# Kernel tuning notes

Measured on AMD Instinct MI355X. Metric: run time of the kernel, lower is better.

The kernel has to match this reference:

```python
import jax, jax.numpy as jnp
import numpy as np

D_MODEL, D_FF, D_NEURON, N_HEADS = 1024, 4096, 128, 8
HEAD_DIM = D_NEURON // N_HEADS
LN_EPS = 1e-5

def gelu(x):
    return jax.nn.gelu(x, approximate=False)  # torch default is exact erf GELU

def setup_inputs() -> dict:
    key = jax.random.key(0)
    ks = jax.random.split(key, 16)
    s = 0.02
    inp = {
        "x": jax.random.normal(ks[0], (2, 2048, D_MODEL), jnp.float32),
        "neuron_patterns": jax.random.normal(ks[1], (D_FF, D_MODEL), jnp.float32) * s,
        "neuron_vecs": jax.random.normal(ks[2], (D_FF, D_NEURON), jnp.float32) * s,
        "neuron_out_dirs": jax.random.normal(ks[3], (D_FF, D_MODEL), jnp.float32) * s,
        "router_w1": jax.random.normal(ks[4], (D_MODEL, D_MODEL), jnp.float32) * s,
        "router_w2": jax.random.normal(ks[5], (D_FF, D_MODEL), jnp.float32) * s,
        "ln_g": jnp.ones((D_MODEL,), jnp.float32),
        "ln_b": jnp.zeros((D_MODEL,), jnp.float32),
        "in_proj_w": jax.random.normal(ks[6], (3 * D_NEURON, D_NEURON), jnp.float32) * s,
        "in_proj_b": jnp.zeros((3 * D_NEURON,), jnp.float32),
        "out_proj_w": jax.random.normal(ks[7], (D_NEURON, D_NEURON), jnp.float32) * s,
        "out_proj_b": jnp.zeros((D_NEURON,), jnp.float32),
        "wp1_w": jax.random.normal(ks[8], (D_NEURON // 2, D_NEURON), jnp.float32) * s,
        "wp1_b": jnp.zeros((D_NEURON // 2,), jnp.float32),
        "wp2_w": jax.random.normal(ks[9], (1, D_NEURON // 2), jnp.float32) * s,
        "wp2_b": jnp.zeros((1,), jnp.float32),
        "top_k": 32,
    }
    return inp

def _forward(x, neuron_patterns, neuron_vecs, neuron_out_dirs, router_w1, router_w2,
             ln_g, ln_b, in_proj_w, in_proj_b, out_proj_w, out_proj_b,
             wp1_w, wp1_b, wp2_w, wp2_b, top_k):
    B, S, D = x.shape
    xf = x.reshape(-1, D)                                  # [N, D]
    # Router (MLP): LayerNorm -> gelu(x @ W1^T) -> @ W2^T
    mu = jnp.mean(xf, axis=-1, keepdims=True)
    var = jnp.mean(jnp.square(xf - mu), axis=-1, keepdims=True)
    xn = (xf - mu) * jax.lax.rsqrt(var + LN_EPS) * ln_g + ln_b
    h = gelu(xn @ router_w1.T)
    scores = h @ router_w2.T                               # [N, d_ff]
    _, idx = jax.lax.top_k(scores, top_k)                  # [N, k]
    pats = neuron_patterns[idx]                            # [N, k, D]
    sems = neuron_vecs[idx]                                # [N, k, dn]
    dirs = neuron_out_dirs[idx]                            # [N, k, D]
    base = gelu(jnp.einsum('nd,nkd->nk', xf, pats))        # [N, k]
    # Small self-attention over the k gathered neuron semantics (eval: no dropout)
    qkv = sems @ in_proj_w.T + in_proj_b                   # [N, k, 3*dn]
    q, kk, v = jnp.split(qkv, 3, axis=-1)
    N, K = q.shape[0], q.shape[1]
    q = q.reshape(N, K, N_HEADS, HEAD_DIM)
    kk = kk.reshape(N, K, N_HEADS, HEAD_DIM)
    v = v.reshape(N, K, N_HEADS, HEAD_DIM)
    att = jnp.einsum('nqhd,nkhd->nhqk', q, kk) / jnp.sqrt(jnp.float32(HEAD_DIM))
    att = jax.nn.softmax(att, axis=-1)
    ao = jnp.einsum('nhqk,nkhd->nqhd', att, v).reshape(N, K, D_NEURON)
    attended = ao @ out_proj_w.T + out_proj_b              # [N, k, dn]
    # Gate: sigmoid(MLP(attended)) -> [N, k, 1]
    sw = jax.nn.sigmoid(gelu(attended @ wp1_w.T + wp1_b) @ wp2_w.T + wp2_b)
    final = base[..., None] * sw                           # [N, k, 1]
    out = jnp.einsum('nko,nkd->nd', final, dirs)           # sum over k neurons
    return out.reshape(B, S, D)

def reference(x, neuron_patterns, neuron_vecs, neuron_out_dirs, router_w1, router_w2,
              ln_g, ln_b, in_proj_w, in_proj_b, out_proj_w, out_proj_b,
              wp1_w, wp1_b, wp2_w, wp2_b, top_k):
    return _forward(x, neuron_patterns, neuron_vecs, neuron_out_dirs, router_w1, router_w2,
                    ln_g, ln_b, in_proj_w, in_proj_b, out_proj_w, out_proj_b,
                    wp1_w, wp1_b, wp2_w, wp2_b, top_k)
```

## Files before the change

kernel.cpp:

```cpp
#include <hip/hip_runtime.h>
#include <math.h>

#define N_TOK 4096
#define DM 1024
#define DFF 4096
#define DN 128
#define NH 8
#define HD 16
#define KSEL 32
#define KCAND 48
#define KMAX 64

typedef __attribute__((ext_vector_type(4))) float floatx4;
typedef __attribute__((ext_vector_type(8))) short short8;
typedef __attribute__((ext_vector_type(8))) unsigned short ushort8v;
typedef __attribute__((ext_vector_type(4))) unsigned short ushort4v;

__device__ __forceinline__ float gelu_f(float x) {
  return 0.5f * x * (1.0f + erff(x * 0.70710678118654752440f));
}
__device__ __forceinline__ float bf2f(unsigned short u) {
  union { unsigned int i; float f; } v; v.i = ((unsigned int)u) << 16; return v.f;
}
__device__ __forceinline__ unsigned short f2bf(float f) {
  unsigned int x = __float_as_uint(f);
  unsigned int r = (x + 0x7fffu + ((x >> 16) & 1u)) >> 16;
  return (unsigned short)r;
}
__device__ __forceinline__ void split3(float v, unsigned short& h, unsigned short& m,
                                       unsigned short& lo) {
  h = f2bf(v);
  float r1 = v - bf2f(h);
  m = f2bf(r1);
  float r2 = r1 - bf2f(m);
  lo = f2bf(r2);
}

__global__ __launch_bounds__(256) void ln3_kernel(const float* __restrict__ x,
    const float* __restrict__ g, const float* __restrict__ b,
    unsigned short* __restrict__ xh, unsigned short* __restrict__ xm,
    unsigned short* __restrict__ xl) {
  int n = blockIdx.x, tid = threadIdx.x;
  const float* row = x + (size_t)n * DM;
  float s = 0.f, sq = 0.f;
  for (int i = tid; i < DM; i += 256) { float v = row[i]; s += v; sq += v * v; }
  for (int off = 32; off; off >>= 1) { s += __shfl_down(s, off); sq += __shfl_down(sq, off); }
  __shared__ float ss[4], ssq[4];
  __shared__ float s_mu, s_rs;
  int wid = tid >> 6;
  if ((tid & 63) == 0) { ss[wid] = s; ssq[wid] = sq; }
  __syncthreads();
  if (tid == 0) {
    float S = ss[0] + ss[1] + ss[2] + ss[3];
    float Q = ssq[0] + ssq[1] + ssq[2] + ssq[3];
    float mu = S * (1.f / DM);
    float var = Q * (1.f / DM) - mu * mu;
    s_mu = mu; s_rs = rsqrtf(var + 1e-5f);
  }
  __syncthreads();
  float mu = s_mu, rs = s_rs;
  size_t base = (size_t)n * DM;
  for (int i = tid; i < DM; i += 256) {
    float v = (row[i] - mu) * rs * g[i] + b[i];
    unsigned short h, m, lo;
    split3(v, h, m, lo);
    xh[base + i] = h; xm[base + i] = m; xl[base + i] = lo;
  }
}

__global__ __launch_bounds__(256) void cvt_split3(const float* __restrict__ in,
    unsigned short* __restrict__ oh, unsigned short* __restrict__ om,
    unsigned short* __restrict__ ol) {
  int i = (blockIdx.x * 256 + threadIdx.x) * 4;
  float4 v = *(const float4*)(in + i);
  unsigned short h0, m0, l0, h1, m1, l1, h2, m2, l2, h3, m3, l3;
  split3(v.x, h0, m0, l0);
  split3(v.y, h1, m1, l1);
  split3(v.z, h2, m2, l2);
  split3(v.w, h3, m3, l3);
  ushort4v hh = {h0, h1, h2, h3};
  ushort4v mm = {m0, m1, m2, m3};
  ushort4v ll = {l0, l1, l2, l3};
  *(ushort4v*)(oh + i) = hh;
  *(ushort4v*)(om + i) = mm;
  *(ushort4v*)(ol + i) = ll;
}

__global__ __launch_bounds__(256) void cvt_bf16(const float* __restrict__ in,
    unsigned short* __restrict__ out) {
  int i = (blockIdx.x * 256 + threadIdx.x) * 4;
  float4 v = *(const float4*)(in + i);
  ushort4v o = {f2bf(v.x), f2bf(v.y), f2bf(v.z), f2bf(v.w)};
  *(ushort4v*)(out + i) = o;
}

__global__ __launch_bounds__(256, 1) void gemm1s(
    const unsigned short* __restrict__ Ah_, const unsigned short* __restrict__ Am_,
    const unsigned short* __restrict__ Al_, const unsigned short* __restrict__ Bh_,
    const unsigned short* __restrict__ Bm_, const unsigned short* __restrict__ Bl_,
    float* __restrict__ H, unsigned short* __restrict__ Hb) {
  __shared__ short Ahs[128 * 32], Ams[128 * 32], Als[128 * 32];
  __shared__ short Bhs[128 * 32], Bms[128 * 32], Bls[128 * 32];
  const int K = 1024;
  const int N = DM;
  int tid = threadIdx.x;
  int w = tid >> 6, l = tid & 63;
  size_t brow = (size_t)blockIdx.y * 128;
  size_t bcol = (size_t)blockIdx.x * 128;

  int r0 = w * 32 + (l >> 2);
  int g0 = (l & 3) ^ ((r0 >> 1) & 3);
  size_t oA0 = (brow + r0) * (size_t)K + g0 * 8;
  size_t oA1 = (brow + r0 + 16) * (size_t)K + g0 * 8;
  size_t oB0 = (bcol + r0) * (size_t)K + g0 * 8;
  size_t oB1 = (bcol + r0 + 16) * (size_t)K + g0 * 8;
  const short* gAh0 = (const short*)Ah_ + oA0; const short* gAh1 = (const short*)Ah_ + oA1;
  const short* gAm0 = (const short*)Am_ + oA0; const short* gAm1 = (const short*)Am_ + oA1;
  const short* gAl0 = (const short*)Al_ + oA0; const short* gAl1 = (const short*)Al_ + oA1;
  const short* gBh0 = (const short*)Bh_ + oB0; const short* gBh1 = (const short*)Bh_ + oB1;
  const short* gBm0 = (const short*)Bm_ + oB0; const short* gBm1 = (const short*)Bm_ + oB1;
  const short* gBl0 = (const short*)Bl_ + oB0; const short* gBl1 = (const short*)Bl_ + oB1;
  short* lAh = &Ahs[w * 1024]; short* lAm = &Ams[w * 1024]; short* lAl = &Als[w * 1024];
  short* lBh = &Bhs[w * 1024]; short* lBm = &Bms[w * 1024]; short* lBl = &Bls[w * 1024];

  const short8 *pah[4], *pam[4], *pal[4], *pbh[4], *pbm[4], *pbl[4];
#pragma unroll
  for (int i = 0; i < 4; i++) {
    int m = (w >> 1) * 64 + i * 16 + (l & 15);
    int slot = m * 4 + ((l >> 4) ^ ((m >> 1) & 3));
    pah[i] = (const short8*)&Ahs[slot * 8];
    pam[i] = (const short8*)&Ams[slot * 8];
    pal[i] = (const short8*)&Als[slot * 8];
    int nn = (w & 1) * 64 + i * 16 + (l & 15);
    int slotb = nn * 4 + ((l >> 4) ^ ((nn >> 1) & 3));
    pbh[i] = (const short8*)&Bhs[slotb * 8];
    pbm[i] = (const short8*)&Bms[slotb * 8];
    pbl[i] = (const short8*)&Bls[slotb * 8];
  }

  floatx4 acc[4][4];
#pragma unroll
  for (int i = 0; i < 4; i++)
#pragma unroll
    for (int j = 0; j < 4; j++) acc[i][j] = (floatx4){0.f, 0.f, 0.f, 0.f};

#define GLD(GP, LB) \
  __builtin_amdgcn_global_load_lds((const __attribute__((address_space(1))) unsigned int*)(GP), \
                                   (__attribute__((address_space(3))) unsigned int*)(LB), 16, 0, 0)

  for (int k0 = 0; k0 < K; k0 += 32) {
    __syncthreads();
    GLD(gAh0 + k0, lAh); GLD(gAh1 + k0, lAh + 512);
    GLD(gAm0 + k0, lAm); GLD(gAm1 + k0, lAm + 512);
    GLD(gAl0 + k0, lAl); GLD(gAl1 + k0, lAl + 512);
    GLD(gBh0 + k0, lBh); GLD(gBh1 + k0, lBh + 512);
    GLD(gBm0 + k0, lBm); GLD(gBm1 + k0, lBm + 512);
    GLD(gBl0 + k0, lBl); GLD(gBl1 + k0, lBl + 512);
    __syncthreads();
    short8 ah[4], am[4], al[4], bh[4], bm[4], bl[4];
#pragma unroll
    for (int i = 0; i < 4; i++) {
      ah[i] = *pah[i]; am[i] = *pam[i]; al[i] = *pal[i];
      bh[i] = *pbh[i]; bm[i] = *pbm[i]; bl[i] = *pbl[i];
    }
#pragma unroll
    for (int i = 0; i < 4; i++)
#pragma unroll
      for (int j = 0; j < 4; j++)
        acc[i][j] = __builtin_amdgcn_mfma_f32_16x16x32_bf16(ah[i], bh[j], acc[i][j], 0, 0, 0);
#pragma unroll
    for (int i = 0; i < 4; i++)
#pragma unroll
      for (int j = 0; j < 4; j++)
        acc[i][j] = __builtin_amdgcn_mfma_f32_16x16x32_bf16(am[i], bh[j], acc[i][j], 0, 0, 0);
#pragma unroll
    for (int i = 0; i < 4; i++)
#pragma unroll
      for (int j = 0; j < 4; j++)
        acc[i][j] = __builtin_amdgcn_mfma_f32_16x16x32_bf16(ah[i], bm[j], acc[i][j], 0, 0, 0);
#pragma unroll
    for (int i = 0; i < 4; i++)
#pragma unroll
      for (int j = 0; j < 4; j++)
        acc[i][j] = __builtin_amdgcn_mfma_f32_16x16x32_bf16(al[i], bh[j], acc[i][j], 0, 0, 0);
#pragma unroll
    for (int i = 0; i < 4; i++)
#pragma unroll
      for (int j = 0; j < 4; j++)
        acc[i][j] = __builtin_amdgcn_mfma_f32_16x16x32_bf16(ah[i], bl[j], acc[i][j], 0, 0, 0);
#pragma unroll
    for (int i = 0; i < 4; i++)
#pragma unroll
      for (int j = 0; j < 4; j++)
        acc[i][j] = __builtin_amdgcn_mfma_f32_16x16x32_bf16(am[i], bm[j], acc[i][j], 0, 0, 0);
  }
#undef GLD

#pragma unroll
  for (int i = 0; i < 4; i++) {
#pragma unroll
    for (int j = 0; j < 4; j++) {
#pragma unroll
      for (int r = 0; r < 4; r++) {
        size_t row = brow + (w >> 1) * 64 + i * 16 + (l >> 4) * 4 + r;
        size_t col = bcol + (w & 1) * 64 + j * 16 + (l & 15);
        float v = gelu_f(acc[i][j][r]);
        H[row * N + col] = v;
        Hb[row * N + col] = f2bf(v);
      }
    }
  }
}

__global__ __launch_bounds__(256) void gemm_bf(const unsigned short* __restrict__ Ah,
    const unsigned short* __restrict__ Bh, unsigned short* __restrict__ C) {
  __shared__ short Asd[128 * 32];
  __shared__ short Bsd[128 * 32];
  const int K = 1024;
  int tid = threadIdx.x;
  int w = tid >> 6, l = tid & 63;
  size_t brow = (size_t)blockIdx.y * 128;
  size_t bcol = (size_t)blockIdx.x * 128;
  const short* Ab = (const short*)Ah + brow * K;
  const short* Bb = (const short*)Bh + bcol * K;

  int r0 = w * 32 + (l >> 2);
  int g0 = (l & 3) ^ ((r0 >> 1) & 3);
  const short* Ag0 = Ab + (size_t)r0 * K + g0 * 8;
  const short* Ag1 = Ab + (size_t)(r0 + 16) * K + g0 * 8;
  const short* Bg0 = Bb + (size_t)r0 * K + g0 * 8;
  const short* Bg1 = Bb + (size_t)(r0 + 16) * K + g0 * 8;
  short* ALds0 = &Asd[w * 1024];
  short* ALds1 = &Asd[w * 1024 + 512];
  short* BLds0 = &Bsd[w * 1024];
  short* BLds1 = &Bsd[w * 1024 + 512];

  const short8* aptr[4];
  const short8* bptr[4];
#pragma unroll
  for (int i = 0; i < 4; i++) {
    int m = (w >> 1) * 64 + i * 16 + (l & 15);
    int slot = m * 4 + ((l >> 4) ^ ((m >> 1) & 3));
    aptr[i] = (const short8*)&Asd[slot * 8];
    int n = (w & 1) * 64 + i * 16 + (l & 15);
    int slotb = n * 4 + ((l >> 4) ^ ((n >> 1) & 3));
    bptr[i] = (const short8*)&Bsd[slotb * 8];
  }

  floatx4 acc[4][4];
#pragma unroll
  for (int i = 0; i < 4; i++)
#pragma unroll
    for (int j = 0; j < 4; j++) acc[i][j] = (floatx4){0.f, 0.f, 0.f, 0.f};

  for (int k0 = 0; k0 < K; k0 += 32) {
    __syncthreads();
    __builtin_amdgcn_global_load_lds((const __attribute__((address_space(1))) unsigned int*)(Ag0 + k0),
                                     (__attribute__((address_space(3))) unsigned int*)ALds0, 16, 0, 0);
    __builtin_amdgcn_global_load_lds((const __attribute__((address_space(1))) unsigned int*)(Ag1 + k0),
                                     (__attribute__((address_space(3))) unsigned int*)ALds1, 16, 0, 0);
    __builtin_amdgcn_global_load_lds((const __attribute__((address_space(1))) unsigned int*)(Bg0 + k0),
                                     (__attribute__((address_space(3))) unsigned int*)BLds0, 16, 0, 0);
    __builtin_amdgcn_global_load_lds((const __attribute__((address_space(1))) unsigned int*)(Bg1 + k0),
                                     (__attribute__((address_space(3))) unsigned int*)BLds1, 16, 0, 0);
    __syncthreads();
    short8 a[4], b[4];
#pragma unroll
    for (int i = 0; i < 4; i++) a[i] = *aptr[i];
#pragma unroll
    for (int j = 0; j < 4; j++) b[j] = *bptr[j];
#pragma unroll
    for (int i = 0; i < 4; i++)
#pragma unroll
      for (int j = 0; j < 4; j++)
        acc[i][j] = __builtin_amdgcn_mfma_f32_16x16x32_bf16(a[i], b[j], acc[i][j], 0, 0, 0);
  }

#pragma unroll
  for (int i = 0; i < 4; i++) {
#pragma unroll
    for (int j = 0; j < 4; j++) {
#pragma unroll
      for (int r = 0; r < 4; r++) {
        size_t row = brow + (w >> 1) * 64 + i * 16 + (l >> 4) * 4 + r;
        size_t col = bcol + (w & 1) * 64 + j * 16 + (l & 15);
        C[row * DFF + col] = f2bf(acc[i][j][r]);
      }
    }
  }
}

__global__ __launch_bounds__(256) void topk2_kernel(const unsigned short* __restrict__ scores,
    int* __restrict__ cand, int* __restrict__ cnt) {
  int wv = threadIdx.x >> 6, l = threadIdx.x & 63;
  int n = blockIdx.x * 4 + wv;
  const ushort8v* row = (const ushort8v*)(scores + (size_t)n * DFF);
  unsigned short key[64];
#pragma unroll
  for (int i = 0; i < 8; i++) {
    ushort8v v = row[l * 8 + i];
#pragma unroll
    for (int e = 0; e < 8; e++) {
      unsigned short u = v[e];
      key[i * 8 + e] = (u & 0x8000u) ? (unsigned short)(~u)
                                     : (unsigned short)(u | 0x8000u);
    }
  }
  unsigned int prefix = 0;
#pragma unroll
  for (int bit = 15; bit >= 0; bit--) {
    unsigned int probe = prefix | (1u << bit);
    int c = 0;
#pragma unroll
    for (int i = 0; i < 64; i++) c += (key[i] >= probe) ? 1 : 0;
#pragma unroll
    for (int s = 1; s < 64; s <<= 1) c += __shfl_xor(c, s);
    if (c >= KCAND) prefix = probe;
  }
  unsigned short thr = (unsigned short)prefix;
  unsigned long long ltmask = (1ull << l) - 1ull;
  int base = 0;
  int* outp = cand + (size_t)n * KMAX;
#pragma unroll
  for (int i = 0; i < 64; i++) {
    bool p = key[i] >= thr;
    unsigned long long m = __ballot(p);
    if (p) {
      int pos = base + __popcll(m & ltmask);
      if (pos < KMAX) outp[pos] = l * 64 + i;
    }
    base += __popcll(m);
  }
  if (l == 0) cnt[n] = base < KMAX ? base : KMAX;
}

__global__ __launch_bounds__(256) void rescore_kernel(const float* __restrict__ h,
    const float* __restrict__ w2f, const int* __restrict__ cand,
    const int* __restrict__ cnt, int* __restrict__ idx32) {
  __shared__ float sh[DM];
  __shared__ float sc[KMAX];
  __shared__ int sidx[KMAX];
  __shared__ int s_cnt;
  int n = blockIdx.x, tid = threadIdx.x;
  *(float4*)&sh[tid * 4] = *(const float4*)(h + (size_t)n * DM + tid * 4);
  if (tid == 0) s_cnt = cnt[n];
  if (tid < KMAX) { sidx[tid] = cand[(size_t)n * KMAX + tid]; sc[tid] = -INFINITY; }
  __syncthreads();
  int cntv = s_cnt;
  int w = tid >> 6, lane = tid & 63;
  for (int c = w; c < cntv; c += 4) {
    const float4* row = (const float4*)(w2f + (size_t)sidx[c] * DM);
    const float4* hp = (const float4*)sh;
    float s = 0.f;
#pragma unroll
    for (int t = 0; t < 4; t++) {
      float4 wv = row[t * 64 + lane];
      float4 hv = hp[t * 64 + lane];
      s = fmaf(wv.x, hv.x, s); s = fmaf(wv.y, hv.y, s);
      s = fmaf(wv.z, hv.z, s); s = fmaf(wv.w, hv.w, s);
    }
    for (int off = 32; off; off >>= 1) s += __shfl_xor(s, off);
    if (lane == 0) sc[c] = s;
  }
  __syncthreads();
  if (tid < cntv) {
    float st = sc[tid]; int it = sidx[tid];
    int rank = 0;
    for (int j = 0; j < KMAX; j++) {
      float sj = sc[j];
      rank += (sj > st) || (sj == st && sidx[j] < it);
    }
    if (rank < KSEL) idx32[(size_t)n * KSEL + rank] = it;
  }
}

__global__ __launch_bounds__(384) void qkvtab_kernel(const float* __restrict__ nv,
    const float* __restrict__ ipw, const float* __restrict__ ipb,
    unsigned short* __restrict__ tab) {
  __shared__ float s_nv[8 * 128];
  int f0 = blockIdx.x * 8;
  int tid = threadIdx.x;
  for (int i = tid; i < 8 * 128; i += 384) s_nv[i] = nv[(size_t)f0 * 128 + i];
  __syncthreads();
  int row = tid;
  float bias = ipb[row];
  float acc[8];
#pragma unroll
  for (int ff = 0; ff < 8; ff++) acc[ff] = bias;
  const float* wr = ipw + (size_t)row * 128;
  for (int c = 0; c < 128; c++) {
    float w = wr[c];
#pragma unroll
    for (int ff = 0; ff < 8; ff++) acc[ff] = fmaf(s_nv[ff * 128 + c], w, acc[ff]);
  }
#pragma unroll
  for (int ff = 0; ff < 8; ff++) tab[(size_t)(f0 + ff) * 384 + row] = f2bf(acc[ff]);
}

#define AOS 132
__global__ __launch_bounds__(256) void tail4_kernel(
    const float* __restrict__ xf, const float* __restrict__ pats,
    const float* __restrict__ dirs, const unsigned short* __restrict__ qtab_b,
    const int* __restrict__ idxs,
    const unsigned short* __restrict__ opwb, const float* __restrict__ opb,
    const unsigned short* __restrict__ w1b, const float* __restrict__ b1,
    const float* __restrict__ w2, const float* __restrict__ b2,
    float* __restrict__ out) {
  __shared__ unsigned short s_kv[2 * 32 * 128];
  __shared__ float s_x[1024];
  __shared__ unsigned short s_ao[32 * AOS];
  __shared__ float s_base[32];
  __shared__ float s_coef[32];
  __shared__ int s_idx[32];
  unsigned short* s_k = s_kv;
  unsigned short* s_v = s_kv + 32 * 128;
  unsigned short* s_at = s_kv;

  int n = blockIdx.x, tid = threadIdx.x;
  int w = tid >> 6, l = tid & 63;

  if (tid < 32) s_idx[tid] = idxs[(size_t)n * 32 + tid];
  *(float4*)&s_x[tid * 4] = *(const float4*)(xf + (size_t)n * DM + tid * 4);
  __syncthreads();

#pragma unroll
  for (int p = 0; p < 4; p++) {
    int i = p * 256 + tid;
    int j = i >> 5, c = i & 31;
    int half = c >> 4, cc = c & 15;
    ushort8v v = *(const ushort8v*)(qtab_b + (size_t)s_idx[j] * 384 + 128 + half * 128 + cc * 8);
    *(ushort8v*)&s_kv[half * 4096 + j * 128 + cc * 8] = v;
  }

  {
    int j = tid >> 3, g = tid & 7;
    const float4* pr = (const float4*)(pats + (size_t)s_idx[j] * DM);
    const float4* xp = (const float4*)s_x;
    float s = 0.f;
#pragma unroll 8
    for (int it = 0; it < 32; it++) {
      float4 pv = pr[it * 8 + g];
      float4 xv = xp[it * 8 + g];
      s = fmaf(pv.x, xv.x, s); s = fmaf(pv.y, xv.y, s);
      s = fmaf(pv.z, xv.z, s); s = fmaf(pv.w, xv.w, s);
    }
    s += __shfl_xor(s, 1);
    s += __shfl_xor(s, 2);
    s += __shfl_xor(s, 4);
    if (g == 0) s_base[j] = gelu_f(s);
  }
  __syncthreads();

  {
    int qj = l & 31;
    int h0 = w * 2 + (l >> 5);
    const ushort8v* qr = (const ushort8v*)(qtab_b + (size_t)s_idx[qj] * 384 + h0 * 16);
    ushort8v q0 = qr[0], q1 = qr[1];
    float q[16];
#pragma unroll
    for (int e = 0; e < 8; e++) { q[e] = bf2f(q0[e]); q[8 + e] = bf2f(q1[e]); }
    float att[32];
#pragma unroll 8
    for (int kj = 0; kj < 32; kj++) {
      const ushort8v* kr = (const ushort8v*)&s_k[kj * 128 + h0 * 16];
      ushort8v k0 = kr[0], k1 = kr[1];
      float s = 0.f;
#pragma unroll
      for (int e = 0; e < 8; e++) s = fmaf(q[e], bf2f(k0[e]), s);
#pragma unroll
      for (int e = 0; e < 8; e++) s = fmaf(q[8 + e], bf2f(k1[e]), s);
      att[kj] = s * 0.25f;
    }
    float m = att[0];
#pragma unroll
    for (int k = 1; k < 32; k++) m = fmaxf(m, att[k]);
    float sum = 0.f;
#pragma unroll
    for (int k = 0; k < 32; k++) { att[k] = expf(att[k] - m); sum += att[k]; }
    float inv = 1.f / sum;
#pragma unroll
    for (int k = 0; k < 32; k++) att[k] *= inv;
    float o[16];
#pragma unroll
    for (int e = 0; e < 16; e++) o[e] = 0.f;
#pragma unroll 8
    for (int kj = 0; kj < 32; kj++) {
      const ushort8v* vr = (const ushort8v*)&s_v[kj * 128 + h0 * 16];
      ushort8v v0 = vr[0], v1 = vr[1];
      float a = att[kj];
#pragma unroll
      for (int e = 0; e < 8; e++) o[e] = fmaf(a, bf2f(v0[e]), o[e]);
#pragma unroll
      for (int e = 0; e < 8; e++) o[8 + e] = fmaf(a, bf2f(v1[e]), o[8 + e]);
    }
    ushort8v o0, o1;
#pragma unroll
    for (int e = 0; e < 8; e++) { o0[e] = f2bf(o[e]); o1[e] = f2bf(o[8 + e]); }
    ushort8v* ao = (ushort8v*)&s_ao[qj * AOS + h0 * 16];
    ao[0] = o0; ao[1] = o1;
  }
  __syncthreads();

  {
    floatx4 acc[4];
#pragma unroll
    for (int nt = 0; nt < 4; nt++) acc[nt] = (floatx4){0.f, 0.f, 0.f, 0.f};
    int rbase = (w & 1) * 16;
    int cblk = (w >> 1) * 4;
#pragma unroll
    for (int kst = 0; kst < 4; kst++) {
      short8 a = *(const short8*)&s_ao[(rbase + (l & 15)) * AOS + kst * 32 + (l >> 4) * 8];
#pragma unroll
      for (int nt = 0; nt < 4; nt++) {
        short8 b = *(const short8*)&opwb[(size_t)((cblk + nt) * 16 + (l & 15)) * 128 + kst * 32 + (l >> 4) * 8];
        acc[nt] = __builtin_amdgcn_mfma_f32_16x16x32_bf16(a, b, acc[nt], 0, 0, 0);
      }
    }
#pragma unroll
    for (int nt = 0; nt < 4; nt++) {
      int col = (cblk + nt) * 16 + (l & 15);
      float bias = opb[col];
#pragma unroll
      for (int r = 0; r < 4; r++) {
        int row = rbase + (l >> 4) * 4 + r;
        s_at[row * AOS + col] = f2bf(acc[nt][r] + bias);
      }
    }
  }
  __syncthreads();

  if (w < 2) {
    floatx4 acc[4];
#pragma unroll
    for (int nt = 0; nt < 4; nt++) acc[nt] = (floatx4){0.f, 0.f, 0.f, 0.f};
#pragma unroll
    for (int kst = 0; kst < 4; kst++) {
      short8 a = *(const short8*)&s_at[(w * 16 + (l & 15)) * AOS + kst * 32 + (l >> 4) * 8];
#pragma unroll
      for (int nt = 0; nt < 4; nt++) {
        short8 b = *(const short8*)&w1b[(size_t)(nt * 16 + (l & 15)) * 128 + kst * 32 + (l >> 4) * 8];
        acc[nt] = __builtin_amdgcn_mfma_f32_16x16x32_bf16(a, b, acc[nt], 0, 0, 0);
      }
    }
    float p[4] = {0.f, 0.f, 0.f, 0.f};
#pragma unroll
    for (int nt = 0; nt < 4; nt++) {
      int col = nt * 16 + (l & 15);
      float bb = b1[col], ww = w2[col];
#pragma unroll
      for (int r = 0; r < 4; r++)
        p[r] = fmaf(gelu_f(acc[nt][r] + bb), ww, p[r]);
    }
#pragma unroll
    for (int r = 0; r < 4; r++) {
      p[r] += __shfl_xor(p[r], 1);
      p[r] += __shfl_xor(p[r], 2);
      p[r] += __shfl_xor(p[r], 4);
      p[r] += __shfl_xor(p[r], 8);
    }
    if ((l & 15) == 0) {
      float b2v = b2[0];
#pragma unroll
      for (int r = 0; r < 4; r++) {
        int row = w * 16 + (l >> 4) * 4 + r;
        float sw = 1.f / (1.f + expf(-(p[r] + b2v)));
        s_coef[row] = s_base[row] * sw;
      }
    }
  }
  __syncthreads();

  {
    int d0 = tid * 4;
    float4 a = {0.f, 0.f, 0.f, 0.f};
#pragma unroll 8
    for (int j = 0; j < 32; j++) {
      float c = s_coef[j];
      float4 dv = *(const float4*)(dirs + (size_t)s_idx[j] * DM + d0);
      a.x = fmaf(c, dv.x, a.x);
      a.y = fmaf(c, dv.y, a.y);
      a.z = fmaf(c, dv.z, a.z);
      a.w = fmaf(c, dv.w, a.w);
    }
    *(float4*)&out[(size_t)n * 1024 + d0] = a;
  }
}

extern "C" void kernel_launch(void* const* d_in, const int* in_sizes, int n_in,
                              void* d_out, int out_size, void* d_ws, size_t ws_size,
                              hipStream_t stream) {
  const float* x    = (const float*)d_in[0];
  const float* pats = (const float*)d_in[1];
  const float* nv   = (const float*)d_in[2];
  const float* dirs = (const float*)d_in[3];
  const float* rw1  = (const float*)d_in[4];
  const float* rw2  = (const float*)d_in[5];
  const float* lng  = (const float*)d_in[6];
  const float* lnb  = (const float*)d_in[7];
  const float* ipw  = (const float*)d_in[8];
  const float* ipb  = (const float*)d_in[9];
  const float* opw  = (const float*)d_in[10];
  const float* opb  = (const float*)d_in[11];
  const float* w1   = (const float*)d_in[12];
  const float* b1   = (const float*)d_in[13];
  const float* w2   = (const float*)d_in[14];
  const float* b2   = (const float*)d_in[15];
  float* out = (float*)d_out;

  const size_t MB = 1u << 20;
  char* ws = (char*)d_ws;
  unsigned short* xnh  = (unsigned short*)(ws + 0);
  unsigned short* xnm  = (unsigned short*)(ws + 8 * MB);
  float* h             = (float*)(ws + 16 * MB);
  unsigned short* sb   = (unsigned short*)(ws + 32 * MB);
  unsigned short* w1h  = (unsigned short*)(ws + 32 * MB);
  unsigned short* w1m  = (unsigned short*)(ws + 34 * MB);
  unsigned short* w1l  = (unsigned short*)(ws + 36 * MB);
  unsigned short* xnl  = (unsigned short*)(ws + 38 * MB);
  unsigned short* qtab = (unsigned short*)(ws + 64 * MB);
  unsigned short* hb   = (unsigned short*)(ws + 67 * MB);
  unsigned short* w2b  = (unsigned short*)(ws + 75 * MB);
  unsigned short* opwb = (unsigned short*)(ws + 99 * MB);
  unsigned short* w1b  = (unsigned short*)(ws + 99 * MB + 64 * 1024);
  int* idx32           = (int*)(ws + 100 * MB);
  int* cand            = (int*)(ws + 101 * MB);
  int* cnt             = (int*)(ws + 102 * MB);

  ln3_kernel<<<N_TOK, 256, 0, stream>>>(x, lng, lnb, xnh, xnm, xnl);
  cvt_split3<<<(DM * DM) / 1024, 256, 0, stream>>>(rw1, w1h, w1m, w1l);
  gemm1s<<<dim3(DM / 128, N_TOK / 128), 256, 0, stream>>>(xnh, xnm, xnl, w1h, w1m, w1l, h, hb);
  cvt_bf16<<<(DFF * DM) / 1024, 256, 0, stream>>>(rw2, w2b);
  cvt_bf16<<<(DN * DN) / 1024, 256, 0, stream>>>(opw, opwb);
  cvt_bf16<<<(DN * DN / 2) / 1024, 256, 0, stream>>>(w1, w1b);
  gemm_bf<<<dim3(DFF / 128, N_TOK / 128), 256, 0, stream>>>(hb, w2b, sb);
  topk2_kernel<<<N_TOK / 4, 256, 0, stream>>>(sb, cand, cnt);
  rescore_kernel<<<N_TOK, 256, 0, stream>>>(h, rw2, cand, cnt, idx32);
  qkvtab_kernel<<<DFF / 8, 384, 0, stream>>>(nv, ipw, ipb, qtab);
  tail4_kernel<<<N_TOK, 256, 0, stream>>>(x, pats, dirs, qtab, idx32,
                                          opwb, opb, w1b, b1, w2, b2, out);
}
```

Baseline: 545.3 us.

## Gather bf16 copies of patterns and out-dirs in tail; stage K/V as fp32

Two new conversion kernels write bf16 copies of neuron_patterns and neuron_out_dirs, and the tail kernel gathers these instead of the fp32 originals. This halves the bytes read in the per-token gathers. K/V are now widened to fp32 once when staged into shared memory, so the attention inner loops no longer convert bf16 per element. The cost is two extra full-matrix conversion passes per call, a doubled shared-memory footprint for K/V that may lower occupancy, and reduced precision in the base activation and the output sum.

```diff
diff --git a/kernel.cpp b/kernel.cpp
--- a/kernel.cpp
+++ b/kernel.cpp
@@ -398,23 +398,23 @@
 }
 
 #define AOS 132
-__global__ __launch_bounds__(256) void tail4_kernel(
-    const float* __restrict__ xf, const float* __restrict__ pats,
-    const float* __restrict__ dirs, const unsigned short* __restrict__ qtab_b,
+__global__ __launch_bounds__(256) void tail5_kernel(
+    const float* __restrict__ xf, const unsigned short* __restrict__ pats_b,
+    const unsigned short* __restrict__ dirs_b, const unsigned short* __restrict__ qtab_b,
     const int* __restrict__ idxs,
     const unsigned short* __restrict__ opwb, const float* __restrict__ opb,
     const unsigned short* __restrict__ w1b, const float* __restrict__ b1,
     const float* __restrict__ w2, const float* __restrict__ b2,
     float* __restrict__ out) {
-  __shared__ unsigned short s_kv[2 * 32 * 128];
+  __shared__ float s_kv[2 * 32 * 128];
   __shared__ float s_x[1024];
   __shared__ unsigned short s_ao[32 * AOS];
   __shared__ float s_base[32];
   __shared__ float s_coef[32];
   __shared__ int s_idx[32];
-  unsigned short* s_k = s_kv;
-  unsigned short* s_v = s_kv + 32 * 128;
-  unsigned short* s_at = s_kv;
+  float* s_k = s_kv;
+  float* s_v = s_kv + 32 * 128;
+  unsigned short* s_at = (unsigned short*)s_kv;
 
   int n = blockIdx.x, tid = threadIdx.x;
   int w = tid >> 6, l = tid & 63;
@@ -429,20 +429,27 @@
     int j = i >> 5, c = i & 31;
     int half = c >> 4, cc = c & 15;
     ushort8v v = *(const ushort8v*)(qtab_b + (size_t)s_idx[j] * 384 + 128 + half * 128 + cc * 8);
-    *(ushort8v*)&s_kv[half * 4096 + j * 128 + cc * 8] = v;
+    float4 f0 = {bf2f(v[0]), bf2f(v[1]), bf2f(v[2]), bf2f(v[3])};
+    float4 f1 = {bf2f(v[4]), bf2f(v[5]), bf2f(v[6]), bf2f(v[7])};
+    float* dst = &s_kv[half * 4096 + j * 128 + cc * 8];
+    *(float4*)dst = f0;
+    *(float4*)(dst + 4) = f1;
   }
 
   {
     int j = tid >> 3, g = tid & 7;
-    const float4* pr = (const float4*)(pats + (size_t)s_idx[j] * DM);
-    const float4* xp = (const float4*)s_x;
+    const ushort8v* pr = (const ushort8v*)(pats_b + (size_t)s_idx[j] * DM);
     float s = 0.f;
-#pragma unroll 8
-    for (int it = 0; it < 32; it++) {
-      float4 pv = pr[it * 8 + g];
-      float4 xv = xp[it * 8 + g];
-      s = fmaf(pv.x, xv.x, s); s = fmaf(pv.y, xv.y, s);
-      s = fmaf(pv.z, xv.z, s); s = fmaf(pv.w, xv.w, s);
+#pragma unroll 4
+    for (int it = 0; it < 16; it++) {
+      int ch = it * 8 + g;
+      ushort8v pv = pr[ch];
+      float4 xv0 = *(const float4*)&s_x[ch * 8];
+      float4 xv1 = *(const float4*)&s_x[ch * 8 + 4];
+      s = fmaf(bf2f(pv[0]), xv0.x, s); s = fmaf(bf2f(pv[1]), xv0.y, s);
+      s = fmaf(bf2f(pv[2]), xv0.z, s); s = fmaf(bf2f(pv[3]), xv0.w, s);
+      s = fmaf(bf2f(pv[4]), xv1.x, s); s = fmaf(bf2f(pv[5]), xv1.y, s);
+      s = fmaf(bf2f(pv[6]), xv1.z, s); s = fmaf(bf2f(pv[7]), xv1.w, s);
     }
     s += __shfl_xor(s, 1);
     s += __shfl_xor(s, 2);
@@ -462,13 +469,17 @@
     float att[32];
 #pragma unroll 8
     for (int kj = 0; kj < 32; kj++) {
-      const ushort8v* kr = (const ushort8v*)&s_k[kj * 128 + h0 * 16];
-      ushort8v k0 = kr[0], k1 = kr[1];
+      const float4* kr = (const float4*)&s_k[kj * 128 + h0 * 16];
+      float4 k0 = kr[0], k1 = kr[1], k2 = kr[2], k3 = kr[3];
       float s = 0.f;
-#pragma unroll
-      for (int e = 0; e < 8; e++) s = fmaf(q[e], bf2f(k0[e]), s);
-#pragma unroll
-      for (int e = 0; e < 8; e++) s = fmaf(q[8 + e], bf2f(k1[e]), s);
+      s = fmaf(q[0], k0.x, s);  s = fmaf(q[1], k0.y, s);
+      s = fmaf(q[2], k0.z, s);  s = fmaf(q[3], k0.w, s);
+      s = fmaf(q[4], k1.x, s);  s = fmaf(q[5], k1.y, s);
+      s = fmaf(q[6], k1.z, s);  s = fmaf(q[7], k1.w, s);
+      s = fmaf(q[8], k2.x, s);  s = fmaf(q[9], k2.y, s);
+      s = fmaf(q[10], k2.z, s); s = fmaf(q[11], k2.w, s);
+      s = fmaf(q[12], k3.x, s); s = fmaf(q[13], k3.y, s);
+      s = fmaf(q[14], k3.z, s); s = fmaf(q[15], k3.w, s);
       att[kj] = s * 0.25f;
     }
     float m = att[0];
@@ -485,13 +496,17 @@
     for (int e = 0; e < 16; e++) o[e] = 0.f;
 #pragma unroll 8
     for (int kj = 0; kj < 32; kj++) {
-      const ushort8v* vr = (const ushort8v*)&s_v[kj * 128 + h0 * 16];
-      ushort8v v0 = vr[0], v1 = vr[1];
+      const float4* vr = (const float4*)&s_v[kj * 128 + h0 * 16];
+      float4 v0 = vr[0], v1 = vr[1], v2 = vr[2], v3 = vr[3];
       float a = att[kj];
-#pragma unroll
-      for (int e = 0; e < 8; e++) o[e] = fmaf(a, bf2f(v0[e]), o[e]);
-#pragma unroll
-      for (int e = 0; e < 8; e++) o[8 + e] = fmaf(a, bf2f(v1[e]), o[8 + e]);
+      o[0] = fmaf(a, v0.x, o[0]);   o[1] = fmaf(a, v0.y, o[1]);
+      o[2] = fmaf(a, v0.z, o[2]);   o[3] = fmaf(a, v0.w, o[3]);
+      o[4] = fmaf(a, v1.x, o[4]);   o[5] = fmaf(a, v1.y, o[5]);
+      o[6] = fmaf(a, v1.z, o[6]);   o[7] = fmaf(a, v1.w, o[7]);
+      o[8] = fmaf(a, v2.x, o[8]);   o[9] = fmaf(a, v2.y, o[9]);
+      o[10] = fmaf(a, v2.z, o[10]); o[11] = fmaf(a, v2.w, o[11]);
+      o[12] = fmaf(a, v3.x, o[12]); o[13] = fmaf(a, v3.y, o[13]);
+      o[14] = fmaf(a, v3.z, o[14]); o[15] = fmaf(a, v3.w, o[15]);
     }
     ushort8v o0, o1;
 #pragma unroll
@@ -576,11 +591,11 @@
 #pragma unroll 8
     for (int j = 0; j < 32; j++) {
       float c = s_coef[j];
-      float4 dv = *(const float4*)(dirs + (size_t)s_idx[j] * DM + d0);
-      a.x = fmaf(c, dv.x, a.x);
-      a.y = fmaf(c, dv.y, a.y);
-      a.z = fmaf(c, dv.z, a.z);
-      a.w = fmaf(c, dv.w, a.w);
+      ushort4v dv = *(const ushort4v*)&dirs_b[(size_t)s_idx[j] * DM + d0];
+      a.x = fmaf(c, bf2f(dv.x), a.x);
+      a.y = fmaf(c, bf2f(dv.y), a.y);
+      a.z = fmaf(c, bf2f(dv.z), a.z);
+      a.w = fmaf(c, bf2f(dv.w), a.w);
     }
     *(float4*)&out[(size_t)n * 1024 + d0] = a;
   }
@@ -620,6 +635,8 @@
   unsigned short* qtab = (unsigned short*)(ws + 64 * MB);
   unsigned short* hb   = (unsigned short*)(ws + 67 * MB);
   unsigned short* w2b  = (unsigned short*)(ws + 75 * MB);
+  unsigned short* patsb= (unsigned short*)(ws + 83 * MB);
+  unsigned short* dirsb= (unsigned short*)(ws + 91 * MB);
   unsigned short* opwb = (unsigned short*)(ws + 99 * MB);
   unsigned short* w1b  = (unsigned short*)(ws + 99 * MB + 64 * 1024);
   int* idx32           = (int*)(ws + 100 * MB);
@@ -630,12 +647,14 @@
   cvt_split3<<<(DM * DM) / 1024, 256, 0, stream>>>(rw1, w1h, w1m, w1l);
   gemm1s<<<dim3(DM / 128, N_TOK / 128), 256, 0, stream>>>(xnh, xnm, xnl, w1h, w1m, w1l, h, hb);
   cvt_bf16<<<(DFF * DM) / 1024, 256, 0, stream>>>(rw2, w2b);
+  cvt_bf16<<<(DFF * DM) / 1024, 256, 0, stream>>>(pats, patsb);
+  cvt_bf16<<<(DFF * DM) / 1024, 256, 0, stream>>>(dirs, dirsb);
   cvt_bf16<<<(DN * DN) / 1024, 256, 0, stream>>>(opw, opwb);
   cvt_bf16<<<(DN * DN / 2) / 1024, 256, 0, stream>>>(w1, w1b);
   gemm_bf<<<dim3(DFF / 128, N_TOK / 128), 256, 0, stream>>>(hb, w2b, sb);
   topk2_kernel<<<N_TOK / 4, 256, 0, stream>>>(sb, cand, cnt);
   rescore_kernel<<<N_TOK, 256, 0, stream>>>(h, rw2, cand, cnt, idx32);
   qkvtab_kernel<<<DFF / 8, 384, 0, stream>>>(nv, ipw, ipb, qtab);
-  tail4_kernel<<<N_TOK, 256, 0, stream>>>(x, pats, dirs, qtab, idx32,
+  tail5_kernel<<<N_TOK, 256, 0, stream>>>(x, patsb, dirsb, qtab, idx32,
                                           opwb, opb, w1b, b1, w2, b2, out);
 }
```

Measured after the change: 555.9 us. Within noise of the previous version (+2.0%).
